# Kernel optimization log

Measured on AMD Instinct MI355X. Metric: run time of the kernel, lower is better.

## Reference

```python
import jax, jax.numpy as jnp
import numpy as np

B, T, C, FFN, N_LAYER, LAYER_ID = 4, 2048, 1024, 4096, 24, 1
EPS = 1e-5


def setup_inputs() -> dict:
    key = jax.random.key(0)
    ks = jax.random.split(key, 10)
    scale = 0.02

    def w(k, shape):
        return (jax.random.normal(k, shape, jnp.float32) * scale)

    # RWKV-4 init formulas for layer_id=1, n_layer=24 (learned params, init per source)
    r01 = LAYER_ID / (N_LAYER - 1)
    r10 = 1.0 - LAYER_ID / N_LAYER
    ddd = np.arange(C, dtype=np.float64) / C
    h = np.arange(C, dtype=np.float64)
    decay = -5.0 + 8.0 * (h / (C - 1)) ** (0.7 + 1.3 * r01)
    zigzag = np.array([(i + 1) % 3 - 1 for i in range(C)], dtype=np.float64) * 0.5
    tfirst = np.log(0.3) + zigzag

    return {
        "x": jax.random.normal(ks[0], (B, T, C), jnp.float32),
        "ln1_w": jnp.ones((C,), jnp.float32), "ln1_b": jnp.zeros((C,), jnp.float32),
        "ln2_w": jnp.ones((C,), jnp.float32), "ln2_b": jnp.zeros((C,), jnp.float32),
        "time_decay": jnp.asarray(decay, jnp.float32),
        "time_first": jnp.asarray(tfirst, jnp.float32),
        "tmk": jnp.asarray(ddd ** r10, jnp.float32),
        "tmv": jnp.asarray(ddd ** r10 + 0.3 * r01, jnp.float32),
        "tmr": jnp.asarray(ddd ** (0.5 * r10), jnp.float32),
        "att_kw": w(ks[1], (C, C)), "att_vw": w(ks[2], (C, C)),
        "att_rw": w(ks[3], (C, C)), "att_ow": w(ks[4], (C, C)),
        "f_tmk": jnp.asarray(ddd ** r10, jnp.float32),
        "f_tmr": jnp.asarray(ddd ** r10, jnp.float32),
        "f_kw": w(ks[5], (FFN, C)), "f_rw": w(ks[6], (C, C)), "f_vw": w(ks[7], (C, FFN)),
    }


def _ln(z, g, b):
    m = jnp.mean(z, axis=-1, keepdims=True)
    v = jnp.mean(jnp.square(z - m), axis=-1, keepdims=True)
    return (z - m) * jax.lax.rsqrt(v + EPS) * g + b


def _shift(z):  # token shift: prepend zero row along T, drop last
    return jnp.pad(z, ((0, 0), (1, 0), (0, 0)))[:, :-1]


def _wkv(time_decay, u, k, v):
    # Numerically-stable RWKV-4 WKV recurrence (log-space max trick).
    # k, v: [B, T, C]; time_decay, u: [C]
    w = -jnp.exp(time_decay)  # per-channel decay (negative)
    kt = jnp.moveaxis(k, 1, 0)  # [T, B, C]
    vt = jnp.moveaxis(v, 1, 0)
    aa = jnp.zeros_like(kt[0])
    bb = jnp.zeros_like(kt[0])
    pp = jnp.full_like(kt[0], -1e38)

    def step(carry, kv):
        aa, bb, pp = carry
        kk, vv = kv
        ww = u + kk
        p = jnp.maximum(pp, ww)
        e1 = jnp.exp(pp - p)
        e2 = jnp.exp(ww - p)
        out = (e1 * aa + e2 * vv) / (e1 * bb + e2)
        ww2 = pp + w
        p2 = jnp.maximum(ww2, kk)
        e1b = jnp.exp(ww2 - p2)
        e2b = jnp.exp(kk - p2)
        return (e1b * aa + e2b * vv, e1b * bb + e2b, p2), out

    _, out = jax.lax.scan(step, (aa, bb, pp), (kt, vt))
    return jnp.moveaxis(out, 0, 1)  # [B, T, C]


def reference(x, ln1_w, ln1_b, ln2_w, ln2_b, time_decay, time_first,
              tmk, tmv, tmr, att_kw, att_vw, att_rw, att_ow,
              f_tmk, f_tmr, f_kw, f_rw, f_vw):
    # --- RWKV_TimeMix (layer_id != 0; protectors are identity in fwd for finite vals) ---
    h = _ln(x, ln1_w, ln1_b)
    hx = _shift(h)
    xk = h * tmk + hx * (1.0 - tmk)
    xv = h * tmv + hx * (1.0 - tmv)
    xr = h * tmr + hx * (1.0 - tmr)
    k = jnp.einsum('btc,dc->btd', xk, att_kw)
    v = jnp.einsum('btc,dc->btd', xv, att_vw)
    sr = jax.nn.sigmoid(jnp.einsum('btc,dc->btd', xr, att_rw))
    rwkv = sr * _wkv(time_decay, time_first, k, v)
    x = x + jnp.einsum('btd,cd->btc', rwkv, att_ow)
    # --- RWKV_ChannelMix ---
    h = _ln(x, ln2_w, ln2_b)
    hx = _shift(h)
    xk = h * f_tmk + hx * (1.0 - f_tmk)
    xr = h * f_tmr + hx * (1.0 - f_tmr)
    kk = jnp.square(jax.nn.relu(jnp.einsum('btc,fc->btf', xk, f_kw)))
    kv = jnp.einsum('btf,cf->btc', kk, f_vw)
    x = x + jax.nn.sigmoid(jnp.einsum('btc,dc->btd', xr, f_rw)) * kv
    return x
```

## Files before the change

kernel.cpp:

```cpp
#include <hip/hip_runtime.h>
#include <cstdint>

#define C_DIM 1024
#define T_DIM 2048
#define B_DIM 4
#define FFN_DIM 4096
#define NROWS (B_DIM * T_DIM)
#define NELEM ((size_t)NROWS * C_DIM)
#define MB ((size_t)1 << 20)
#define NSEG 32
#define SEGL (T_DIM / NSEG)

typedef __bf16 bf16;
typedef _Float16 f16;
typedef __bf16 bf16x4 __attribute__((ext_vector_type(4)));
typedef __bf16 bf16x8 __attribute__((ext_vector_type(8)));
typedef float  floatx4 __attribute__((ext_vector_type(4)));

#define GLDS(g, l) __builtin_amdgcn_global_load_lds(                          \
    (const __attribute__((address_space(1))) void*)(g),                       \
    (__attribute__((address_space(3))) void*)(l), 16, 0, 0)

struct W7 {
    const float* s[7];
    bf16*        d[7];
    int          cum[8];
};

__global__ __launch_bounds__(256) void f2b7_kernel(W7 w)
{
    int id = blockIdx.x * 256 + threadIdx.x;
    int seg = 0;
#pragma unroll
    for (int j = 1; j < 7; ++j) if (id >= w.cum[j]) seg = j;
    int i = id - w.cum[seg];
    float4 v = ((const float4*)w.s[seg])[i];
    bf16x4 o = { (bf16)v.x, (bf16)v.y, (bf16)v.z, (bf16)v.w };
    ((bf16x4*)w.d[seg])[i] = o;
}

template<bool HASV>
__global__ __launch_bounds__(256) void lnmix_kernel(const float* __restrict__ x,
                                                    const float* __restrict__ g,
                                                    const float* __restrict__ b,
                                                    const float* __restrict__ mk,
                                                    const float* __restrict__ mv,
                                                    const float* __restrict__ mr,
                                                    bf16* __restrict__ xk,
                                                    bf16* __restrict__ xv,
                                                    bf16* __restrict__ xr)
{
    int row = blockIdx.x;
    int t   = row & (T_DIM - 1);
    int tid = threadIdx.x;
    size_t i4 = (size_t)row * 256 + tid;

    float4 v  = ((const float4*)x)[i4];
    float4 vp = make_float4(0.f, 0.f, 0.f, 0.f);
    if (t != 0) vp = ((const float4*)x)[i4 - 256];

    float s   = v.x + v.y + v.z + v.w;
    float s2  = v.x * v.x + v.y * v.y + v.z * v.z + v.w * v.w;
    float sp  = vp.x + vp.y + vp.z + vp.w;
    float sp2 = vp.x * vp.x + vp.y * vp.y + vp.z * vp.z + vp.w * vp.w;
    for (int off = 32; off > 0; off >>= 1) {
        s   += __shfl_down(s,   off);
        s2  += __shfl_down(s2,  off);
        sp  += __shfl_down(sp,  off);
        sp2 += __shfl_down(sp2, off);
    }
    __shared__ float red[16];
    int lane = tid & 63, wid = tid >> 6;
    if (lane == 0) { red[wid] = s; red[4 + wid] = s2; red[8 + wid] = sp; red[12 + wid] = sp2; }
    __syncthreads();
    s   = red[0] + red[1] + red[2] + red[3];
    s2  = red[4] + red[5] + red[6] + red[7];
    sp  = red[8] + red[9] + red[10] + red[11];
    sp2 = red[12] + red[13] + red[14] + red[15];

    float mean  = s * (1.0f / C_DIM);
    float inv   = rsqrtf(s2 * (1.0f / C_DIM) - mean * mean + 1e-5f);
    float meanp = sp * (1.0f / C_DIM);
    float invp  = rsqrtf(sp2 * (1.0f / C_DIM) - meanp * meanp + 1e-5f);

    float4 gv = ((const float4*)g)[tid];
    float4 bv = ((const float4*)b)[tid];
    float4 hv, hp;
    hv.x = (v.x - mean) * inv * gv.x + bv.x;
    hv.y = (v.y - mean) * inv * gv.y + bv.y;
    hv.z = (v.z - mean) * inv * gv.z + bv.z;
    hv.w = (v.w - mean) * inv * gv.w + bv.w;
    if (t != 0) {
        hp.x = (vp.x - meanp) * invp * gv.x + bv.x;
        hp.y = (vp.y - meanp) * invp * gv.y + bv.y;
        hp.z = (vp.z - meanp) * invp * gv.z + bv.z;
        hp.w = (vp.w - meanp) * invp * gv.w + bv.w;
    } else {
        hp = make_float4(0.f, 0.f, 0.f, 0.f);
    }

    float4 m1 = ((const float4*)mk)[tid];
    bf16x4 o;
    o.x = (bf16)(hp.x + m1.x * (hv.x - hp.x));
    o.y = (bf16)(hp.y + m1.y * (hv.y - hp.y));
    o.z = (bf16)(hp.z + m1.z * (hv.z - hp.z));
    o.w = (bf16)(hp.w + m1.w * (hv.w - hp.w));
    ((bf16x4*)xk)[i4] = o;

    if (HASV) {
        float4 m2 = ((const float4*)mv)[tid];
        o.x = (bf16)(hp.x + m2.x * (hv.x - hp.x));
        o.y = (bf16)(hp.y + m2.y * (hv.y - hp.y));
        o.z = (bf16)(hp.z + m2.z * (hv.z - hp.z));
        o.w = (bf16)(hp.w + m2.w * (hv.w - hp.w));
        ((bf16x4*)xv)[i4] = o;
    }

    float4 m3 = ((const float4*)mr)[tid];
    o.x = (bf16)(hp.x + m3.x * (hv.x - hp.x));
    o.y = (bf16)(hp.y + m3.y * (hv.y - hp.y));
    o.z = (bf16)(hp.z + m3.z * (hv.z - hp.z));
    o.w = (bf16)(hp.w + m3.w * (hv.w - hp.w));
    ((bf16x4*)xr)[i4] = o;
}

#define EPI_NONE 0
#define EPI_SIG 1
#define EPI_RELU2 2
#define EPI_ADD 3
#define EPI_SCALEADD 4

struct GArgs {
    const bf16*  A[4];
    const bf16*  W[4];
    void*        Y[4];
    const float* X2[4];
    const bf16*  S[4];
    int N[4], K[4], epi[4], outk[4], blk0[4];
    int ng;
};

__global__ __launch_bounds__(256) void gemm_grouped(GArgs G)
{
    __shared__ unsigned short As[128 * 64];
    __shared__ unsigned short Bs[128 * 64];

    int id = blockIdx.x;
    int gi = 0;
#pragma unroll
    for (int j = 1; j < 4; ++j) if (j < G.ng && id >= G.blk0[j]) gi = j;

    const bf16* A = G.A[gi];
    const bf16* W = G.W[gi];
    int N = G.N[gi], K = G.K[gi];
    int lid = id - G.blk0[gi];

    int xcd = lid & 7, r = lid >> 3;
    int m_t = xcd * 8 + (r & 7);
    int n_t = r >> 3;
    int m0 = m_t << 7, n0 = n_t << 7;

    int tid = threadIdx.x;
    int wv = tid >> 6;
    int ln = tid & 63;

    int qsrc = (ln & 7) ^ ((ln >> 3) & 7);
    const bf16* Ag = A + (size_t)(m0 + wv * 8 + (ln >> 3)) * K + qsrc * 8;
    const bf16* Wg = W + (size_t)(n0 + wv * 8 + (ln >> 3)) * K + qsrc * 8;
    size_t row32K = (size_t)32 * K;
    unsigned short* AsW = As + (wv * 8) * 64;
    unsigned short* BsW = Bs + (wv * 8) * 64;

    int wm = (wv & 1) * 64, wn = (wv >> 1) * 64;
    int arow = wm + (ln & 15);
    int brow = wn + (ln & 15);
    int q0 = (ln >> 4) ^ (ln & 7);
    int q1 = ((ln >> 4) + 4) ^ (ln & 7);
    int aoff0 = arow * 64 + q0 * 8, aoff1 = arow * 64 + q1 * 8;
    int boff0 = brow * 64 + q0 * 8, boff1 = brow * 64 + q1 * 8;

    floatx4 acc[4][4] = {};

    for (int k0 = 0; k0 < K; k0 += 64) {
        if (k0) __syncthreads();
#pragma unroll
        for (int j = 0; j < 4; ++j)
            GLDS(Ag + k0 + (size_t)j * row32K, AsW + j * 32 * 64);
#pragma unroll
        for (int j = 0; j < 4; ++j)
            GLDS(Wg + k0 + (size_t)j * row32K, BsW + j * 32 * 64);
        __syncthreads();

        bf16x8 a0[4], a1[4], b0[4], b1[4];
#pragma unroll
        for (int i = 0; i < 4; ++i) {
            a0[i] = *(const bf16x8*)(As + aoff0 + i * 1024);
            a1[i] = *(const bf16x8*)(As + aoff1 + i * 1024);
        }
#pragma unroll
        for (int j = 0; j < 4; ++j) {
            b0[j] = *(const bf16x8*)(Bs + boff0 + j * 1024);
            b1[j] = *(const bf16x8*)(Bs + boff1 + j * 1024);
        }
#pragma unroll
        for (int i = 0; i < 4; ++i)
#pragma unroll
            for (int j = 0; j < 4; ++j)
                acc[i][j] = __builtin_amdgcn_mfma_f32_16x16x32_bf16(a0[i], b0[j], acc[i][j], 0, 0, 0);
#pragma unroll
        for (int i = 0; i < 4; ++i)
#pragma unroll
            for (int j = 0; j < 4; ++j)
                acc[i][j] = __builtin_amdgcn_mfma_f32_16x16x32_bf16(a1[i], b1[j], acc[i][j], 0, 0, 0);
    }

    int epi = G.epi[gi], outk = G.outk[gi];
    const float* X2 = G.X2[gi];
    const bf16*  S  = G.S[gi];
    float* Yf = (float*)G.Y[gi];
    bf16*  Yh = (bf16*)G.Y[gi];
    f16*   Ye = (f16*)G.Y[gi];

    int row0 = (ln >> 4) * 4;
    int colb = n0 + wn + (ln & 15);
#pragma unroll
    for (int i = 0; i < 4; ++i) {
        int gm = m0 + wm + i * 16 + row0;
#pragma unroll
        for (int j = 0; j < 4; ++j) {
            int gn = colb + j * 16;
#pragma unroll
            for (int rr = 0; rr < 4; ++rr) {
                size_t idx = (size_t)(gm + rr) * N + gn;
                float v = acc[i][j][rr];
                if (epi == EPI_SIG)        v = 1.0f / (1.0f + __expf(-v));
                else if (epi == EPI_RELU2) { float t = fmaxf(v, 0.0f); v = t * t; }
                else if (epi == EPI_ADD)   v = X2[idx] + v;
                else if (epi == EPI_SCALEADD) v = X2[idx] + (float)S[idx] * v;
                if (outk == 0)      Yf[idx] = v;
                else if (outk == 1) Yh[idx] = (bf16)v;
                else                Ye[idx] = (f16)v;
            }
        }
    }
}

__global__ __launch_bounds__(256) void wkv_seg(const f16* __restrict__ k,
                                               const f16* __restrict__ v,
                                               const float* __restrict__ decay,
                                               float* __restrict__ sa,
                                               float* __restrict__ sb,
                                               float* __restrict__ sp)
{
    int idx = blockIdx.x * 256 + threadIdx.x;
    int c   = idx & (C_DIM - 1);
    int bs  = idx >> 10;
    int seg = bs & (NSEG - 1);
    int b   = bs >> 5;
    float w = -__expf(decay[c]);
    size_t base = ((size_t)b * T_DIM + (size_t)seg * SEGL) * C_DIM + c;
    float aa = 0.f, bb = 0.f, pp = -1e38f;
    for (int t = 0; t < SEGL; ++t) {
        size_t off = base + (size_t)t * C_DIM;
        float kk = (float)k[off], vv = (float)v[off];
        float ww2 = pp + w;
        float p2  = fmaxf(ww2, kk);
        float e1  = __expf(ww2 - p2);
        float e2  = __expf(kk - p2);
        aa = e1 * aa + e2 * vv;
        bb = e1 * bb + e2;
        pp = p2;
    }
    sa[idx] = aa; sb[idx] = bb; sp[idx] = pp;
}

__global__ __launch_bounds__(256) void wkv_comb(const float* __restrict__ sa,
                                                const float* __restrict__ sb,
                                                const float* __restrict__ sp,
                                                const float* __restrict__ decay,
                                                float* __restrict__ ia,
                                                float* __restrict__ ib,
                                                float* __restrict__ ip)
{
    int idx = blockIdx.x * 256 + threadIdx.x;
    int c = idx & (C_DIM - 1);
    int b = idx >> 10;
    float wL = -__expf(decay[c]) * (float)SEGL;
    float aa = 0.f, bb = 0.f, pp = -1e38f;
    size_t base = (size_t)b * NSEG * C_DIM + c;
    for (int j = 0; j < NSEG; ++j) {
        size_t o = base + (size_t)j * C_DIM;
        ia[o] = aa; ib[o] = bb; ip[o] = pp;
        float a_s = sa[o], b_s = sb[o], p_s = sp[o];
        float pd = pp + wL;
        float pn = fmaxf(pd, p_s);
        float e1 = __expf(pd - pn);
        float e2 = __expf(p_s - pn);
        aa = e1 * aa + e2 * a_s;
        bb = e1 * bb + e2 * b_s;
        pp = pn;
    }
}

__global__ __launch_bounds__(256) void wkv_out(const f16* __restrict__ k,
                                               const f16* __restrict__ v,
                                               const bf16* __restrict__ sr,
                                               const float* __restrict__ decay,
                                               const float* __restrict__ first,
                                               const float* __restrict__ ia,
                                               const float* __restrict__ ib,
                                               const float* __restrict__ ip,
                                               bf16* __restrict__ out)
{
    int idx = blockIdx.x * 256 + threadIdx.x;
    int c   = idx & (C_DIM - 1);
    int bs  = idx >> 10;
    int seg = bs & (NSEG - 1);
    int b   = bs >> 5;
    float w = -__expf(decay[c]);
    float u = first[c];
    float aa = ia[idx], bb = ib[idx], pp = ip[idx];
    size_t base = ((size_t)b * T_DIM + (size_t)seg * SEGL) * C_DIM + c;
    for (int t = 0; t < SEGL; ++t) {
        size_t off = base + (size_t)t * C_DIM;
        float kk = (float)k[off], vv = (float)v[off];
        float ww = u + kk;
        float p  = fmaxf(pp, ww);
        float e1 = __expf(pp - p);
        float e2 = __expf(ww - p);
        float o  = (e1 * aa + e2 * vv) / (e1 * bb + e2);
        out[off] = (bf16)((float)sr[off] * o);
        float ww2 = pp + w;
        float p2  = fmaxf(ww2, kk);
        float e1b = __expf(ww2 - p2);
        float e2b = __expf(kk - p2);
        aa = e1b * aa + e2b * vv;
        bb = e1b * bb + e2b;
        pp = p2;
    }
}

extern "C" void kernel_launch(void* const* d_in, const int* in_sizes, int n_in,
                              void* d_out, int out_size, void* d_ws, size_t ws_size,
                              hipStream_t stream)
{
    const float* x          = (const float*)d_in[0];
    const float* ln1_w      = (const float*)d_in[1];
    const float* ln1_b      = (const float*)d_in[2];
    const float* ln2_w      = (const float*)d_in[3];
    const float* ln2_b      = (const float*)d_in[4];
    const float* time_decay = (const float*)d_in[5];
    const float* time_first = (const float*)d_in[6];
    const float* tmk        = (const float*)d_in[7];
    const float* tmv        = (const float*)d_in[8];
    const float* tmr        = (const float*)d_in[9];
    const float* att_kw     = (const float*)d_in[10];
    const float* att_vw     = (const float*)d_in[11];
    const float* att_rw     = (const float*)d_in[12];
    const float* att_ow     = (const float*)d_in[13];
    const float* f_tmk      = (const float*)d_in[14];
    const float* f_tmr      = (const float*)d_in[15];
    const float* f_kw       = (const float*)d_in[16];
    const float* f_rw       = (const float*)d_in[17];
    const float* f_vw       = (const float*)d_in[18];
    float* out = (float*)d_out;

    char* W8 = (char*)d_ws;
    bf16* kw_b  = (bf16*)(W8 + 0 * MB);
    bf16* vw_b  = (bf16*)(W8 + 2 * MB);
    bf16* rw_b  = (bf16*)(W8 + 4 * MB);
    bf16* ow_b  = (bf16*)(W8 + 6 * MB);
    bf16* fkw_b = (bf16*)(W8 + 8 * MB);
    bf16* frw_b = (bf16*)(W8 + 16 * MB);
    bf16* fvw_b = (bf16*)(W8 + 18 * MB);

    bf16*  xk_b   = (bf16*)(W8 + 26 * MB);
    bf16*  xv_b   = (bf16*)(W8 + 42 * MB);
    bf16*  xr_b   = (bf16*)(W8 + 58 * MB);
    bf16*  rwkv_b = xk_b;
    bf16*  xk2_b  = (bf16*)(W8 + 26 * MB);
    bf16*  xr2_b  = (bf16*)(W8 + 42 * MB);
    bf16*  sr2_b  = (bf16*)(W8 + 58 * MB);
    f16*   kbuf   = (f16*)(W8 + 74 * MB);
    f16*   vbuf   = (f16*)(W8 + 90 * MB);
    bf16*  srb_b  = (bf16*)(W8 + 106 * MB);
    bf16*  kk_b   = (bf16*)(W8 + 122 * MB);

    size_t KB512 = (size_t)512 * 1024;
    float* sc_a = (float*)(W8 + 186 * MB);
    float* sc_b = (float*)(W8 + 186 * MB + 1 * KB512);
    float* sc_p = (float*)(W8 + 186 * MB + 2 * KB512);
    float* in_a = (float*)(W8 + 186 * MB + 3 * KB512);
    float* in_b = (float*)(W8 + 186 * MB + 4 * KB512);
    float* in_p = (float*)(W8 + 186 * MB + 5 * KB512);

    int nC4 = C_DIM * C_DIM / 4, nF4 = FFN_DIM * C_DIM / 4;
    W7 w7;
    const float* srcs[7] = { att_kw, att_vw, att_rw, att_ow, f_kw, f_rw, f_vw };
    bf16*        dsts[7] = { kw_b, vw_b, rw_b, ow_b, fkw_b, frw_b, fvw_b };
    int          cnts[7] = { nC4, nC4, nC4, nC4, nF4, nC4, nF4 };
    int cum = 0;
    for (int i = 0; i < 7; ++i) { w7.s[i] = srcs[i]; w7.d[i] = dsts[i]; w7.cum[i] = cum; cum += cnts[i]; }
    w7.cum[7] = cum;
    f2b7_kernel<<<cum / 256, 256, 0, stream>>>(w7);

    auto mkdesc = [](GArgs& G, int& total, const bf16* A, const bf16* W, void* Y,
                     const float* X2, const bf16* S, int N, int K, int epi, int outk) {
        int i = G.ng;
        G.A[i] = A; G.W[i] = W; G.Y[i] = Y; G.X2[i] = X2; G.S[i] = S;
        G.N[i] = N; G.K[i] = K; G.epi[i] = epi; G.outk[i] = outk;
        G.blk0[i] = total; total += 64 * (N >> 7); G.ng = i + 1;
    };

    int segGrid = B_DIM * NSEG * C_DIM / 256;

    lnmix_kernel<true><<<NROWS, 256, 0, stream>>>(x, ln1_w, ln1_b, tmk, tmv, tmr,
                                                  xk_b, xv_b, xr_b);
    {
        GArgs G = {}; int total = 0;
        mkdesc(G, total, xk_b, kw_b, kbuf,  nullptr, nullptr, C_DIM, C_DIM, EPI_NONE, 2);
        mkdesc(G, total, xv_b, vw_b, vbuf,  nullptr, nullptr, C_DIM, C_DIM, EPI_NONE, 2);
        mkdesc(G, total, xr_b, rw_b, srb_b, nullptr, nullptr, C_DIM, C_DIM, EPI_SIG,  1);
        gemm_grouped<<<total, 256, 0, stream>>>(G);
    }
    wkv_seg<<<segGrid, 256, 0, stream>>>(kbuf, vbuf, time_decay, sc_a, sc_b, sc_p);
    wkv_comb<<<B_DIM * C_DIM / 256, 256, 0, stream>>>(sc_a, sc_b, sc_p, time_decay, in_a, in_b, in_p);
    wkv_out<<<segGrid, 256, 0, stream>>>(kbuf, vbuf, srb_b, time_decay, time_first,
                                         in_a, in_b, in_p, rwkv_b);
    {
        GArgs G = {}; int total = 0;
        mkdesc(G, total, rwkv_b, ow_b, out, x, nullptr, C_DIM, C_DIM, EPI_ADD, 0);
        gemm_grouped<<<total, 256, 0, stream>>>(G);
    }

    lnmix_kernel<false><<<NROWS, 256, 0, stream>>>(out, ln2_w, ln2_b, f_tmk, nullptr, f_tmr,
                                                   xk2_b, nullptr, xr2_b);
    {
        GArgs G = {}; int total = 0;
        mkdesc(G, total, xr2_b, frw_b, sr2_b, nullptr, nullptr, C_DIM,   C_DIM, EPI_SIG,   1);
        mkdesc(G, total, xk2_b, fkw_b, kk_b,  nullptr, nullptr, FFN_DIM, C_DIM, EPI_RELU2, 1);
        gemm_grouped<<<total, 256, 0, stream>>>(G);
    }
    {
        GArgs G = {}; int total = 0;
        mkdesc(G, total, kk_b, fvw_b, out, out, sr2_b, C_DIM, FFN_DIM, EPI_SCALEADD, 0);
        gemm_grouped<<<total, 256, 0, stream>>>(G);
    }
}
```

Before: 568.8 us.

## Double-buffer GEMM LDS with 128x256 tiles and double the WKV segments

Rewrites the grouped GEMM to use 128x256 output tiles with a K-step of 32 and double-buffered LDS, issuing the next stage's global-to-LDS loads before computing on the current buffer. Each wave now holds a 4x8 MFMA accumulator block. The aim is to overlap memory traffic with MFMA work and raise operand reuse. In exchange it uses more accumulator registers, though launch bounds still request two blocks per CU. The WKV scan now uses 64 segments instead of 32, with unroll hints, and the segment scratch buffers are enlarged to match, giving the serial recurrence more parallelism.

Result: slower. 635.3 us (+11.7%).

```diff
diff --git a/kernel.cpp b/kernel.cpp
--- a/kernel.cpp
+++ b/kernel.cpp
@@ -8,7 +8,7 @@
 #define NROWS (B_DIM * T_DIM)
 #define NELEM ((size_t)NROWS * C_DIM)
 #define MB ((size_t)1 << 20)
-#define NSEG 32
+#define NSEG 64
 #define SEGL (T_DIM / NSEG)
 
 typedef __bf16 bf16;
@@ -130,6 +130,8 @@
 #define EPI_ADD 3
 #define EPI_SCALEADD 4
 
+#define LDS_BUF 12288
+
 struct GArgs {
     const bf16*  A[4];
     const bf16*  W[4];
@@ -140,10 +142,9 @@
     int ng;
 };
 
-__global__ __launch_bounds__(256) void gemm_grouped(GArgs G)
-{
-    __shared__ unsigned short As[128 * 64];
-    __shared__ unsigned short Bs[128 * 64];
+__global__ __launch_bounds__(256, 2) void gemm_grouped(GArgs G)
+{
+    __shared__ unsigned short lds[2 * LDS_BUF];
 
     int id = blockIdx.x;
     int gi = 0;
@@ -155,63 +156,70 @@
     int N = G.N[gi], K = G.K[gi];
     int lid = id - G.blk0[gi];
 
-    int xcd = lid & 7, r = lid >> 3;
-    int m_t = xcd * 8 + (r & 7);
-    int n_t = r >> 3;
-    int m0 = m_t << 7, n0 = n_t << 7;
+    int xcd = lid & 7, s = lid >> 3;
+    int m_t = xcd * 8 + (s & 7);
+    int n_t = s >> 3;
+    int m0 = m_t << 7, n0 = n_t << 8;
 
     int tid = threadIdx.x;
     int wv = tid >> 6;
     int ln = tid & 63;
 
-    int qsrc = (ln & 7) ^ ((ln >> 3) & 7);
-    const bf16* Ag = A + (size_t)(m0 + wv * 8 + (ln >> 3)) * K + qsrc * 8;
-    const bf16* Wg = W + (size_t)(n0 + wv * 8 + (ln >> 3)) * K + qsrc * 8;
-    size_t row32K = (size_t)32 * K;
-    unsigned short* AsW = As + (wv * 8) * 64;
-    unsigned short* BsW = Bs + (wv * 8) * 64;
-
-    int wm = (wv & 1) * 64, wn = (wv >> 1) * 64;
-    int arow = wm + (ln & 15);
-    int brow = wn + (ln & 15);
-    int q0 = (ln >> 4) ^ (ln & 7);
-    int q1 = ((ln >> 4) + 4) ^ (ln & 7);
-    int aoff0 = arow * 64 + q0 * 8, aoff1 = arow * 64 + q1 * 8;
-    int boff0 = brow * 64 + q0 * 8, boff1 = brow * 64 + q1 * 8;
-
-    floatx4 acc[4][4] = {};
-
-    for (int k0 = 0; k0 < K; k0 += 64) {
-        if (k0) __syncthreads();
-#pragma unroll
-        for (int j = 0; j < 4; ++j)
-            GLDS(Ag + k0 + (size_t)j * row32K, AsW + j * 32 * 64);
-#pragma unroll
-        for (int j = 0; j < 4; ++j)
-            GLDS(Wg + k0 + (size_t)j * row32K, BsW + j * 32 * 64);
+    int qsrc = ((ln & 3) - ((ln >> 3) & 3)) & 3;
+    const bf16* Ag = A + (size_t)(m0 + wv * 16 + (ln >> 2)) * K + qsrc * 8;
+    const bf16* Wg = W + (size_t)(n0 + wv * 16 + (ln >> 2)) * K + qsrc * 8;
+    size_t row64K = (size_t)64 * K;
+    int stgbase = (wv * 16) * 32;
+
+    int wm = (wv & 1) * 64, wn = (wv >> 1) * 128;
+    int aoffL[4], boffL[8];
+    {
+        int rA = ln & 15;
+        int q  = ln >> 4;
+        int sw = ((q + ((ln >> 1) & 3)) & 3) * 8;
+#pragma unroll
+        for (int i = 0; i < 4; ++i) aoffL[i] = (wm + rA + i * 16) * 32 + sw;
+#pragma unroll
+        for (int j = 0; j < 8; ++j) boffL[j] = 4096 + (wn + rA + j * 16) * 32 + sw;
+    }
+
+    floatx4 acc[4][8] = {};
+
+    int niter = K >> 5;
+    {
+        unsigned short* buf = lds;
+#pragma unroll
+        for (int r = 0; r < 2; ++r)
+            GLDS(Ag + (size_t)r * row64K, buf + stgbase + r * 64 * 32);
+#pragma unroll
+        for (int r = 0; r < 4; ++r)
+            GLDS(Wg + (size_t)r * row64K, buf + 4096 + stgbase + r * 64 * 32);
+    }
+
+    for (int it = 0; it < niter; ++it) {
         __syncthreads();
-
-        bf16x8 a0[4], a1[4], b0[4], b1[4];
-#pragma unroll
-        for (int i = 0; i < 4; ++i) {
-            a0[i] = *(const bf16x8*)(As + aoff0 + i * 1024);
-            a1[i] = *(const bf16x8*)(As + aoff1 + i * 1024);
+        unsigned short* cur = lds + (it & 1) * LDS_BUF;
+        if (it + 1 < niter) {
+            unsigned short* nxt = lds + ((it + 1) & 1) * LDS_BUF;
+            size_t k0 = (size_t)(it + 1) << 5;
+#pragma unroll
+            for (int r = 0; r < 2; ++r)
+                GLDS(Ag + k0 + (size_t)r * row64K, nxt + stgbase + r * 64 * 32);
+#pragma unroll
+            for (int r = 0; r < 4; ++r)
+                GLDS(Wg + k0 + (size_t)r * row64K, nxt + 4096 + stgbase + r * 64 * 32);
         }
-#pragma unroll
-        for (int j = 0; j < 4; ++j) {
-            b0[j] = *(const bf16x8*)(Bs + boff0 + j * 1024);
-            b1[j] = *(const bf16x8*)(Bs + boff1 + j * 1024);
-        }
+
+        bf16x8 af[4], bf_[8];
+#pragma unroll
+        for (int i = 0; i < 4; ++i) af[i] = *(const bf16x8*)(cur + aoffL[i]);
+#pragma unroll
+        for (int j = 0; j < 8; ++j) bf_[j] = *(const bf16x8*)(cur + boffL[j]);
 #pragma unroll
         for (int i = 0; i < 4; ++i)
 #pragma unroll
-            for (int j = 0; j < 4; ++j)
-                acc[i][j] = __builtin_amdgcn_mfma_f32_16x16x32_bf16(a0[i], b0[j], acc[i][j], 0, 0, 0);
-#pragma unroll
-        for (int i = 0; i < 4; ++i)
-#pragma unroll
-            for (int j = 0; j < 4; ++j)
-                acc[i][j] = __builtin_amdgcn_mfma_f32_16x16x32_bf16(a1[i], b1[j], acc[i][j], 0, 0, 0);
+            for (int j = 0; j < 8; ++j)
+                acc[i][j] = __builtin_amdgcn_mfma_f32_16x16x32_bf16(af[i], bf_[j], acc[i][j], 0, 0, 0);
     }
 
     int epi = G.epi[gi], outk = G.outk[gi];
@@ -227,7 +235,7 @@
     for (int i = 0; i < 4; ++i) {
         int gm = m0 + wm + i * 16 + row0;
 #pragma unroll
-        for (int j = 0; j < 4; ++j) {
+        for (int j = 0; j < 8; ++j) {
             int gn = colb + j * 16;
 #pragma unroll
             for (int rr = 0; rr < 4; ++rr) {
@@ -256,10 +264,11 @@
     int c   = idx & (C_DIM - 1);
     int bs  = idx >> 10;
     int seg = bs & (NSEG - 1);
-    int b   = bs >> 5;
+    int b   = bs >> 6;
     float w = -__expf(decay[c]);
     size_t base = ((size_t)b * T_DIM + (size_t)seg * SEGL) * C_DIM + c;
     float aa = 0.f, bb = 0.f, pp = -1e38f;
+#pragma unroll 4
     for (int t = 0; t < SEGL; ++t) {
         size_t off = base + (size_t)t * C_DIM;
         float kk = (float)k[off], vv = (float)v[off];
@@ -316,11 +325,12 @@
     int c   = idx & (C_DIM - 1);
     int bs  = idx >> 10;
     int seg = bs & (NSEG - 1);
-    int b   = bs >> 5;
+    int b   = bs >> 6;
     float w = -__expf(decay[c]);
     float u = first[c];
     float aa = ia[idx], bb = ib[idx], pp = ip[idx];
     size_t base = ((size_t)b * T_DIM + (size_t)seg * SEGL) * C_DIM + c;
+#pragma unroll 4
     for (int t = 0; t < SEGL; ++t) {
         size_t off = base + (size_t)t * C_DIM;
         float kk = (float)k[off], vv = (float)v[off];
@@ -386,13 +396,12 @@
     bf16*  srb_b  = (bf16*)(W8 + 106 * MB);
     bf16*  kk_b   = (bf16*)(W8 + 122 * MB);
 
-    size_t KB512 = (size_t)512 * 1024;
     float* sc_a = (float*)(W8 + 186 * MB);
-    float* sc_b = (float*)(W8 + 186 * MB + 1 * KB512);
-    float* sc_p = (float*)(W8 + 186 * MB + 2 * KB512);
-    float* in_a = (float*)(W8 + 186 * MB + 3 * KB512);
-    float* in_b = (float*)(W8 + 186 * MB + 4 * KB512);
-    float* in_p = (float*)(W8 + 186 * MB + 5 * KB512);
+    float* sc_b = (float*)(W8 + 187 * MB);
+    float* sc_p = (float*)(W8 + 188 * MB);
+    float* in_a = (float*)(W8 + 189 * MB);
+    float* in_b = (float*)(W8 + 190 * MB);
+    float* in_p = (float*)(W8 + 191 * MB);
 
     int nC4 = C_DIM * C_DIM / 4, nF4 = FFN_DIM * C_DIM / 4;
     W7 w7;
@@ -409,7 +418,7 @@
         int i = G.ng;
         G.A[i] = A; G.W[i] = W; G.Y[i] = Y; G.X2[i] = X2; G.S[i] = S;
         G.N[i] = N; G.K[i] = K; G.epi[i] = epi; G.outk[i] = outk;
-        G.blk0[i] = total; total += 64 * (N >> 7); G.ng = i + 1;
+        G.blk0[i] = total; total += 64 * (N >> 8); G.ng = i + 1;
     };
 
     int segGrid = B_DIM * NSEG * C_DIM / 256;
```
